# Performance work log

Measured on AMD Instinct MI355X. Metric: run time of the kernel, lower is better.

Reference implementation:

```python
import jax, jax.numpy as jnp
import numpy as np

E, D, H, B = 8, 64, 512, 32768  # n_experts, state_dim, hidden width, batch
IN = D + 3  # x, t, sin(omega*t), cos(omega*t)


def setup_inputs() -> dict:
    key = jax.random.key(0)
    ks = jax.random.split(key, 12)
    s = 0.02
    return {
        "t": jax.random.uniform(ks[0], (1,), dtype=jnp.float32),
        "x": jax.random.normal(ks[1], (B, D), dtype=jnp.float32),
        "expert_weights": jax.random.uniform(ks[2], (B, E), dtype=jnp.float32),
        "omega": jnp.arange(1, E + 1, dtype=jnp.float32),  # omega_i = i+1
        "W1": jax.random.normal(ks[3], (E, H, IN), dtype=jnp.float32) * s,
        "b1": jnp.zeros((E, H), dtype=jnp.float32),
        "W2": jax.random.normal(ks[4], (E, H, H), dtype=jnp.float32) * s,
        "b2": jnp.zeros((E, H), dtype=jnp.float32),
        "W3": jax.random.normal(ks[5], (E, H, H), dtype=jnp.float32) * s,
        "b3": jnp.zeros((E, H), dtype=jnp.float32),
        "W4": jax.random.normal(ks[6], (E, D, H), dtype=jnp.float32) * s,
        "b4": jnp.zeros((E, D), dtype=jnp.float32),
    }


def reference(t, x, expert_weights, omega, W1, b1, W2, b2, W3, b3, W4, b4):
    # Dense path of ExpertODEEnsemble.forward: all experts active.
    nB = x.shape[0]
    tb = jnp.broadcast_to(t, (nB,))                       # (B,)
    wt = omega[:, None] * tb[None, :]                     # (E, B)
    # Per-expert inputs: [x, t, sin(wt), cos(wt)] -> (E, B, D+3)
    xe = jnp.broadcast_to(x[None], (E, nB, D))
    te = jnp.broadcast_to(tb[None, :, None], (E, nB, 1))
    inp = jnp.concatenate([xe, te, jnp.sin(wt)[..., None], jnp.cos(wt)[..., None]], axis=-1)
    h = jnp.tanh(jnp.einsum('ebi,ehi->ebh', inp, W1) + b1[:, None, :])
    h = jnp.tanh(jnp.einsum('ebh,egh->ebg', h, W2) + b2[:, None, :])
    h = jnp.tanh(jnp.einsum('ebh,egh->ebg', h, W3) + b3[:, None, :])
    dyn = jnp.einsum('ebh,edh->ebd', h, W4) + b4[:, None, :]   # (E, B, D)
    # Weighted combine: sum_e w[b,e] * dyn[e,b,:]
    dx_dt = jnp.einsum('be,ebd->bd', expert_weights, dyn)
    return dx_dt
```

## Files before the change

kernel.cpp:

```cpp
#include <hip/hip_runtime.h>
#include <hip/hip_bf16.h>


typedef unsigned short ushort_t;
typedef unsigned int u32;
typedef unsigned long long u64;
typedef __attribute__((ext_vector_type(8))) short short8;
typedef __attribute__((ext_vector_type(4))) float floatx4;
typedef __attribute__((ext_vector_type(16))) float floatx16;
typedef __attribute__((ext_vector_type(4))) int intx4;

#define W1A_OFF 0u
#define W2A_OFF 524288u
#define W3A_OFF 4718592u
#define W4A_OFF 8912896u
#define XB_OFF  9437184u
#define B1E_OFF 13631488u

#define SLOTB 16384
#define SYNC_OFF 147456
#define SMEM_SZ 147552

static __device__ __forceinline__ u32 pk2bf(float a, float b) {
  union { __hip_bfloat162 h; u32 u; } v;
  v.h = __float22bfloat162_rn(make_float2(a, b));
  return v.u;
}

static __device__ __forceinline__ float pade_tanh(float x) {
  float x2 = x * x;
  float num = __builtin_fmaf(x2, __builtin_fmaf(x2, 1.0f, 105.0f), 945.0f);
  float den = __builtin_fmaf(x2, __builtin_fmaf(x2, 15.0f, 420.0f), 945.0f);
  return x * num * __builtin_amdgcn_rcpf(den);
}

static __device__ __forceinline__ floatx16 mfma32(short8 a, short8 b, floatx16 c) {
  return __builtin_amdgcn_mfma_f32_32x32x16_bf16(a, b, c, 0, 0, 0);
}

static __device__ __forceinline__ int slot9(int g, int b) {
  int s = g + b;
  if (s >= 9) s -= 9;
  return s * SLOTB;
}

static __device__ __forceinline__ void waitge(const int* p, int tgt) {
  while (*(volatile const int*)p < tgt) __builtin_amdgcn_s_sleep(1);
  __asm__ __volatile__("" ::: "memory");
}

static __device__ __forceinline__ void waitge4(const int* p, int tgt) {
  for (;;) {
    __asm__ __volatile__("" ::: "memory");
    intx4 v = *(const intx4*)p;
    if (v[0] >= tgt && v[1] >= tgt && v[2] >= tgt && v[3] >= tgt) break;
    __builtin_amdgcn_s_sleep(1);
  }
  __asm__ __volatile__("" ::: "memory");
}

static __device__ __forceinline__ void guard_grp(const int* grp, int w, int base) {
  int tg0 = base + ((0 - w - 1) & 7) + 1;
  int tg1 = base + ((1 - w - 1) & 7) + 1;
  int tg2 = base + ((2 - w - 1) & 7) + 1;
  int tg3 = base + ((3 - w - 1) & 7) + 1;
  int tg4 = base + ((4 - w - 1) & 7) + 1;
  int tg5 = base + ((5 - w - 1) & 7) + 1;
  int tg6 = base + ((6 - w - 1) & 7) + 1;
  int tg7 = base + ((7 - w - 1) & 7) + 1;
  for (;;) {
    __asm__ __volatile__("" ::: "memory");
    intx4 a = *(const intx4*)grp;
    intx4 b = *(const intx4*)(grp + 4);
    if (a[0] >= tg0 && a[1] >= tg1 && a[2] >= tg2 && a[3] >= tg3 &&
        b[0] >= tg4 && b[1] >= tg5 && b[2] >= tg6 && b[3] >= tg7) break;
    __builtin_amdgcn_s_sleep(1);
  }
  __asm__ __volatile__("" ::: "memory");
}

static __device__ __forceinline__ void bump(int* p, int lane) {
  __asm__ __volatile__("s_waitcnt lgkmcnt(0)" ::: "memory");
  if (lane == 0) atomicAdd(p, 1);
}

static __device__ __forceinline__ void bump_sig(int* p, int lane) {
  __builtin_amdgcn_sched_barrier(0);
  if (lane == 0) atomicAdd(p, 1);
}

__global__ __launch_bounds__(256) void prep_kernel(
    const float* __restrict__ t, const float* __restrict__ x,
    const float* __restrict__ omega, const float* __restrict__ W1,
    const float* __restrict__ b1, const float* __restrict__ W2,
    const float* __restrict__ W3, const float* __restrict__ W4,
    char* __restrict__ ws) {
  int i = blockIdx.x * 256 + threadIdx.x;
  if (i < 32768) {
    int e = i >> 12, d = i & 4095;
    int lane = d & 63, q = d >> 6;
    int ol = q & 1, kc = (q >> 1) & 3, w = q >> 3;
    int outr = w * 64 + ol * 32 + (lane & 31);
    int kg = kc * 2 + (lane >> 5);
    const float* s = W1 + (e * 512 + outr) * 67 + kg * 8;
    ((intx4*)(ws + W1A_OFF))[i] = (intx4){
        (int)pk2bf(s[0], s[1]), (int)pk2bf(s[2], s[3]),
        (int)pk2bf(s[4], s[5]), (int)pk2bf(s[6], s[7])};
    return;
  }
  i -= 32768;
  if (i < 262144) {
    int e = i >> 15, d = i & 32767;
    int lane = d & 63, q = d >> 6;
    int ol = q & 1, kc = (q >> 1) & 31, w = q >> 6;
    int outr = w * 64 + ol * 32 + (lane & 31);
    int kg = kc * 2 + (lane >> 5);
    const floatx4* s = (const floatx4*)(W2 + ((e << 9) + outr) * 512 + (kg << 3));
    floatx4 lo = s[0], hi = s[1];
    ((intx4*)(ws + W2A_OFF))[i] = (intx4){
        (int)pk2bf(lo[0], lo[1]), (int)pk2bf(lo[2], lo[3]),
        (int)pk2bf(hi[0], hi[1]), (int)pk2bf(hi[2], hi[3])};
    return;
  }
  i -= 262144;
  if (i < 262144) {
    int e = i >> 15, d = i & 32767;
    int lane = d & 63, q = d >> 6;
    int ol = q & 1, kc = (q >> 1) & 31, w = q >> 6;
    int outr = w * 64 + ol * 32 + (lane & 31);
    int kg = kc * 2 + (lane >> 5);
    const floatx4* s = (const floatx4*)(W3 + ((e << 9) + outr) * 512 + (kg << 3));
    floatx4 lo = s[0], hi = s[1];
    ((intx4*)(ws + W3A_OFF))[i] = (intx4){
        (int)pk2bf(lo[0], lo[1]), (int)pk2bf(lo[2], lo[3]),
        (int)pk2bf(hi[0], hi[1]), (int)pk2bf(hi[2], hi[3])};
    return;
  }
  i -= 262144;
  if (i < 32768) {
    int e = i >> 12, d = i & 4095;
    int lane = d & 63, q = d >> 6;
    int kc = q & 31, o4 = q >> 5;
    int outr = o4 * 32 + (lane & 31);
    int kg = kc * 2 + (lane >> 5);
    const floatx4* s = (const floatx4*)(W4 + ((e << 6) + outr) * 512 + (kg << 3));
    floatx4 lo = s[0], hi = s[1];
    ((intx4*)(ws + W4A_OFF))[i] = (intx4){
        (int)pk2bf(lo[0], lo[1]), (int)pk2bf(lo[2], lo[3]),
        (int)pk2bf(hi[0], hi[1]), (int)pk2bf(hi[2], hi[3])};
    return;
  }
  i -= 32768;
  if (i < 262144) {
    const floatx4* s = (const floatx4*)(x + i * 8);
    floatx4 lo = s[0], hi = s[1];
    ((intx4*)(ws + XB_OFF))[i] = (intx4){
        (int)pk2bf(lo[0], lo[1]), (int)pk2bf(lo[2], lo[3]),
        (int)pk2bf(hi[0], hi[1]), (int)pk2bf(hi[2], hi[3])};
    return;
  }
  i -= 262144;
  if (i < 4096) {
    float tv = t[0];
    int e = i >> 9;
    float om = omega[e];
    ((float*)(ws + B1E_OFF))[i] = b1[i] + tv * W1[i * 67 + 64]
        + sinf(om * tv) * W1[i * 67 + 65] + cosf(om * tv) * W1[i * 67 + 66];
  }
}


static __device__ __forceinline__ void epi_write(
    floatx16 acc[2][4], char* __restrict__ act, int wbyte, int r31, int q1) {
#pragma unroll
  for (int ol = 0; ol < 2; ++ol) {
#pragma unroll
    for (int g = 0; g < 4; ++g) {
      int ko = ol * 4 + g;
      char* base = act + wbyte + (ko >> 1) * 4096
                   + (((ko & 1) * 32 + r31) << 4) + q1 * 8;
#pragma unroll
      for (int nt = 0; nt < 4; ++nt) {
        float v0 = pade_tanh(acc[ol][nt][4 * g + 0]);
        float v1 = pade_tanh(acc[ol][nt][4 * g + 1]);
        float v2 = pade_tanh(acc[ol][nt][4 * g + 2]);
        float v3 = pade_tanh(acc[ol][nt][4 * g + 3]);
        u32 lo = pk2bf(v0, v1), hi = pk2bf(v2, v3);
        *(u64*)(base + nt * 1024) = ((u64)hi << 32) | lo;
      }
    }
  }
}

static __device__ __forceinline__ void mlp_l1(
    char* __restrict__ act, int* pub, int* l4c, int* grp,
    int lane, int w, int q1, int r31,
    const char* __restrict__ Abase, const float* __restrict__ bias,
    const char* __restrict__ xl, int wbyte, int e) {
  const int voff = lane * 16;
  const char* ap = Abase + w * 8192 + voff;

  floatx16 acc[2][4];
#pragma unroll
  for (int ol = 0; ol < 2; ++ol) {
    int fe0 = w * 64 + ol * 32 + 4 * q1;
#pragma unroll
    for (int g = 0; g < 4; ++g) {
      floatx4 bv = *(const floatx4*)(bias + fe0 + 8 * g);
#pragma unroll
      for (int nt = 0; nt < 4; ++nt) {
        acc[ol][nt][4 * g + 0] = bv[0];
        acc[ol][nt][4 * g + 1] = bv[1];
        acc[ol][nt][4 * g + 2] = bv[2];
        acc[ol][nt][4 * g + 3] = bv[3];
      }
    }
  }
  short8 b0 = *(const short8*)(xl);
  short8 b1v = *(const short8*)(xl + 4096);
  short8 b2 = *(const short8*)(xl + 8192);
  short8 b3 = *(const short8*)(xl + 12288);
  short8 a0 = *(const short8*)(ap);
  short8 a1 = *(const short8*)(ap + 1024);

#pragma unroll
  for (int j = 0; j < 4; ++j) {
    int kcn = (j < 3) ? (j + 1) : 3;
    const char* xn = xl + kcn * 32;
    const char* apn = (j < 3) ? (ap + 2048) : ap;
    short8 an0 = *(const short8*)(apn);
    short8 an1 = *(const short8*)(apn + 1024);
    short8 bn0 = *(const short8*)(xn);
    short8 bn1 = *(const short8*)(xn + 4096);
    short8 bn2 = *(const short8*)(xn + 8192);
    short8 bn3 = *(const short8*)(xn + 12288);
    __builtin_amdgcn_s_setprio(1);
    acc[0][0] = mfma32(a0, b0, acc[0][0]);
    acc[0][1] = mfma32(a0, b1v, acc[0][1]);
    acc[0][2] = mfma32(a0, b2, acc[0][2]);
    acc[0][3] = mfma32(a0, b3, acc[0][3]);
    acc[1][0] = mfma32(a1, b0, acc[1][0]);
    acc[1][1] = mfma32(a1, b1v, acc[1][1]);
    acc[1][2] = mfma32(a1, b2, acc[1][2]);
    acc[1][3] = mfma32(a1, b3, acc[1][3]);
    __builtin_amdgcn_s_setprio(0);
    a0 = an0; a1 = an1;
    b0 = bn0; b1v = bn1; b2 = bn2; b3 = bn3;
    ap = apn;
  }
  if (e > 0) {
    if (w < 7) waitge4(l4c + ((w + 1) >> 2) * 4, e);
    else       guard_grp(grp, w, 16 * e - 8);
  }
  epi_write(acc, act, wbyte, r31, q1);
  bump(pub + w, lane);
}

static __device__ __forceinline__ void mlp_mid(
    char* __restrict__ act, int* pub, int* grp, int lane, int w, int q1, int r31,
    const char* __restrict__ Abase, const float* __restrict__ bias,
    int pub_tgt, int rbase9, int wbyte, int gmode, int garg,
    const int* __restrict__ l4p) {
  const int voff = lane * 16;
  const char* spA = Abase + w * 65536 + voff;

  floatx16 acc[2][4];
#pragma unroll
  for (int ol = 0; ol < 2; ++ol) {
    int fe0 = w * 64 + ol * 32 + 4 * q1;
#pragma unroll
    for (int g = 0; g < 4; ++g) {
      floatx4 bv = *(const floatx4*)(bias + fe0 + 8 * g);
#pragma unroll
      for (int nt = 0; nt < 4; ++nt) {
        acc[ol][nt][4 * g + 0] = bv[0];
        acc[ol][nt][4 * g + 1] = bv[1];
        acc[ol][nt][4 * g + 2] = bv[2];
        acc[ol][nt][4 * g + 3] = bv[3];
      }
    }
  }
  const char* gb = act + slot9(w, rbase9) + voff;
  const char* ap = spA + (4 * w) * 2048;
  short8 b0 = *(const short8*)(gb);
  short8 b1v = *(const short8*)(gb + 1024);
  short8 b2 = *(const short8*)(gb + 2048);
  short8 b3 = *(const short8*)(gb + 3072);
  short8 a0 = *(const short8*)(ap);
  short8 a1 = *(const short8*)(ap + 1024);

#pragma unroll 1
  for (int i = 0; i < 8; ++i) {
#pragma unroll
    for (int j = 0; j < 4; ++j) {
      const char* apn;
      const char* gbn = gb;
      const char* bsl;
      if (j < 3) {
        apn = ap + 2048;
        bsl = gb + (j + 1) * 4096;
      } else if (i < 7) {
        int g2 = (w - i - 1) & 7;
        waitge(pub + g2, pub_tgt);
        gbn = act + slot9(g2, rbase9) + voff;
        apn = spA + (4 * g2) * 2048;
        bsl = gbn;
      } else {
        apn = ap; bsl = gb;
      }
      short8 an0 = *(const short8*)(apn);
      short8 an1 = *(const short8*)(apn + 1024);
      short8 bn0 = *(const short8*)(bsl);
      short8 bn1 = *(const short8*)(bsl + 1024);
      short8 bn2 = *(const short8*)(bsl + 2048);
      short8 bn3 = *(const short8*)(bsl + 3072);
      __builtin_amdgcn_s_setprio(1);
      acc[0][0] = mfma32(a0, b0, acc[0][0]);
      acc[0][1] = mfma32(a0, b1v, acc[0][1]);
      acc[0][2] = mfma32(a0, b2, acc[0][2]);
      acc[0][3] = mfma32(a0, b3, acc[0][3]);
      acc[1][0] = mfma32(a1, b0, acc[1][0]);
      acc[1][1] = mfma32(a1, b1v, acc[1][1]);
      acc[1][2] = mfma32(a1, b2, acc[1][2]);
      acc[1][3] = mfma32(a1, b3, acc[1][3]);
      __builtin_amdgcn_s_setprio(0);
      a0 = an0; a1 = an1;
      b0 = bn0; b1v = bn1; b2 = bn2; b3 = bn3;
      ap = apn; gb = gbn;
    }
    bump_sig(grp + w, lane);
  }

  if (gmode == 1)      guard_grp(grp, w, garg);
  else if (gmode == 2) waitge4(l4p, garg);
  epi_write(acc, act, wbyte, r31, q1);
  bump(pub + w, lane);
}

extern "C" __global__ __launch_bounds__(512) void fused_kernel(
    const char* __restrict__ ws, const float* __restrict__ b2,
    const float* __restrict__ b3, const float* __restrict__ b4,
    const float* __restrict__ ew, float* __restrict__ out) {
  extern __shared__ char smem[];
  char* act = smem;
  int* l4c = (int*)(smem + SYNC_OFF);
  int* pub = l4c + 8;
  int* grp = l4c + 16;

  const int t = threadIdx.x, lane = t & 63, w = t >> 6;
  const int q1 = lane >> 5, r31 = lane & 31;
  const int row0 = blockIdx.x << 7;
  const int voff = lane * 16;

  if (t < 24) ((int*)(smem + SYNC_OFF))[t] = 0;
  __syncthreads();

  for (int i = (7 - w) * 7; i > 0; --i) __builtin_amdgcn_s_sleep(1);

  const char* xl = (const char*)ws + XB_OFF + (size_t)row0 * 128
                   + r31 * 128 + q1 * 16;

  const int rt = w & 3, kh = w >> 2;
  const int row_l4 = row0 + rt * 32 + r31;
  floatx16 oacc[2] = {};

  for (int e = 0; e < 8; ++e) {
    int l0 = 3 * e;
    int s1 = (l0 + 1) % 9, s2 = (l0 + 2) % 9, s3 = (l0 + 3) % 9;

    mlp_l1(act, pub, l4c, grp, lane, w, q1, r31,
           (const char*)ws + W1A_OFF + e * 65536,
           (const float*)(ws + B1E_OFF) + e * 512, xl, slot9(w, s1), e);
    mlp_mid(act, pub, grp, lane, w, q1, r31,
            (const char*)ws + W2A_OFF + e * 524288, b2 + e * 512,
            3 * e + 1, s1, slot9(w, s2),
            (w < 7) ? 1 : ((e > 0) ? 2 : 0),
            (w < 7) ? 16 * e : e, l4c);
    mlp_mid(act, pub, grp, lane, w, q1, r31,
            (const char*)ws + W3A_OFF + e * 524288, b3 + e * 512,
            3 * e + 2, s2, slot9(w, s3),
            1, (w < 7) ? 16 * e + 8 : 16 * e, l4c);

    {
      const char* spA4 = (const char*)ws + W4A_OFF + e * 65536 + voff;
      const float sc = ew[row_l4 * 8 + e];
      floatx16 acc4[2] = {};
      int g = 4 * kh + 3;
      waitge(pub + g, 3 * e + 3);
      const char* agb = spA4 + (4 * g) * 1024;
      const char* gb = act + slot9(g, s3) + rt * 1024 + voff;
      short8 a0 = *(const short8*)(agb);
      short8 a1 = *(const short8*)(agb + 32768);
      short8 b = *(const short8*)(gb);
#pragma unroll 1
      for (int gl = 0; gl < 4; ++gl) {
#pragma unroll
        for (int j = 0; j < 4; ++j) {
          const char* agn = agb;
          const char* gbn = gb;
          const char* asl; const char* bsl;
          if (j < 3) {
            asl = agb + (j + 1) * 1024;
            bsl = gb + (j + 1) * 4096;
          } else if (gl < 3) {
            int g2 = g - 1;
            waitge(pub + g2, 3 * e + 3);
            agn = spA4 + (4 * g2) * 1024;
            gbn = act + slot9(g2, s3) + rt * 1024 + voff;
            asl = agn; bsl = gbn;
          } else {
            asl = agb; bsl = gb;
          }
          short8 an0 = *(const short8*)(asl);
          short8 an1 = *(const short8*)(asl + 32768);
          short8 bn = *(const short8*)(bsl);
          __builtin_amdgcn_s_setprio(1);
          acc4[0] = mfma32(a0, b, acc4[0]);
          acc4[1] = mfma32(a1, b, acc4[1]);
          __builtin_amdgcn_s_setprio(0);
          a0 = an0; a1 = an1; b = bn;
          agb = agn; gb = gbn;
        }
        g = g - 1;
      }
      bump_sig(l4c + w, lane);
      if (kh == 0) {
        const float* bp = b4 + e * 64;
#pragma unroll
        for (int ol = 0; ol < 2; ++ol) {
          int fe0 = ol * 32 + 4 * q1;
#pragma unroll
          for (int g2 = 0; g2 < 4; ++g2) {
            floatx4 bv = *(const floatx4*)(bp + fe0 + 8 * g2);
            oacc[ol][4 * g2 + 0] += sc * (acc4[ol][4 * g2 + 0] + bv[0]);
            oacc[ol][4 * g2 + 1] += sc * (acc4[ol][4 * g2 + 1] + bv[1]);
            oacc[ol][4 * g2 + 2] += sc * (acc4[ol][4 * g2 + 2] + bv[2]);
            oacc[ol][4 * g2 + 3] += sc * (acc4[ol][4 * g2 + 3] + bv[3]);
          }
        }
      } else {
#pragma unroll
        for (int ol = 0; ol < 2; ++ol)
#pragma unroll
          for (int i = 0; i < 16; ++i) oacc[ol][i] += sc * acc4[ol][i];
      }
    }
  }

  __syncthreads();
  if (kh == 1) {
#pragma unroll
    for (int ol = 0; ol < 2; ++ol)
#pragma unroll
      for (int g = 0; g < 4; ++g) {
        floatx4 p = {oacc[ol][4 * g + 0], oacc[ol][4 * g + 1],
                     oacc[ol][4 * g + 2], oacc[ol][4 * g + 3]};
        *(floatx4*)(act + rt * 8192 + ol * 4096 + g * 1024 + lane * 16) = p;
      }
  }
  __syncthreads();
  if (kh == 0) {
    float* orow = out + (size_t)row_l4 * 64;
#pragma unroll
    for (int ol = 0; ol < 2; ++ol)
#pragma unroll
      for (int g = 0; g < 4; ++g) {
        floatx4 p = *(const floatx4*)(act + rt * 8192 + ol * 4096 + g * 1024 + lane * 16);
        floatx4 v = {oacc[ol][4 * g + 0] + p[0], oacc[ol][4 * g + 1] + p[1],
                     oacc[ol][4 * g + 2] + p[2], oacc[ol][4 * g + 3] + p[3]};
        *(floatx4*)(orow + ol * 32 + 8 * g + 4 * q1) = v;
      }
  }
}

extern "C" void kernel_launch(void* const* d_in, const int* in_sizes, int n_in,
                              void* d_out, int out_size, void* d_ws, size_t ws_size,
                              hipStream_t stream) {
  const float* t  = (const float*)d_in[0];
  const float* x  = (const float*)d_in[1];
  const float* ew = (const float*)d_in[2];
  const float* om = (const float*)d_in[3];
  const float* W1 = (const float*)d_in[4];
  const float* b1 = (const float*)d_in[5];
  const float* W2 = (const float*)d_in[6];
  const float* b2 = (const float*)d_in[7];
  const float* W3 = (const float*)d_in[8];
  const float* b3 = (const float*)d_in[9];
  const float* W4 = (const float*)d_in[10];
  const float* b4 = (const float*)d_in[11];
  char* ws = (char*)d_ws;
  float* out = (float*)d_out;
  (void)in_sizes; (void)n_in; (void)ws_size; (void)out_size;

  static int smem_set = 0;
  if (!smem_set) {
    hipFuncSetAttribute((const void*)fused_kernel,
                        hipFuncAttributeMaxDynamicSharedMemorySize, SMEM_SZ);
    smem_set = 1;
  }
  prep_kernel<<<3344, 256, 0, stream>>>(t, x, om, W1, b1, W2, W3, W4, ws);
  fused_kernel<<<256, 512, SMEM_SZ, stream>>>(ws, b2, b3, b4, ew, out);
}
```

Measured before the change: 461.3 us.

## Stage x tile into LDS once and shrink activation ring to eight slots

Loads the block's bf16 x tile into LDS once at kernel start with global_load_lds, so layer 1 of every expert reads x from LDS instead of re-reading it from global memory eight times. To free the LDS for this, the activation ring buffer drops from nine slots to eight, using a mask instead of a modulo. The cross-wave guard logic is simplified to match. The smaller ring changes slot reuse distances, which could add stalls or hazards between layers.

```diff
diff --git a/kernel.cpp b/kernel.cpp
--- a/kernel.cpp
+++ b/kernel.cpp
@@ -18,6 +18,7 @@
 #define B1E_OFF 13631488u
 
 #define SLOTB 16384
+#define X_OFF_L 131072
 #define SYNC_OFF 147456
 #define SMEM_SZ 147552
 
@@ -34,14 +35,18 @@
   return x * num * __builtin_amdgcn_rcpf(den);
 }
 
+static __device__ __forceinline__ void ald16(const void* g, void* l) {
+  __builtin_amdgcn_global_load_lds((__attribute__((address_space(1))) void*)g,
+                                   (__attribute__((address_space(3))) void*)l,
+                                   16, 0, 0);
+}
+
 static __device__ __forceinline__ floatx16 mfma32(short8 a, short8 b, floatx16 c) {
   return __builtin_amdgcn_mfma_f32_32x32x16_bf16(a, b, c, 0, 0, 0);
 }
 
-static __device__ __forceinline__ int slot9(int g, int b) {
-  int s = g + b;
-  if (s >= 9) s -= 9;
-  return s * SLOTB;
+static __device__ __forceinline__ int slot8(int g, int b) {
+  return ((g + b) & 7) * SLOTB;
 }
 
 static __device__ __forceinline__ void waitge(const int* p, int tgt) {
@@ -193,10 +198,10 @@
 }
 
 static __device__ __forceinline__ void mlp_l1(
-    char* __restrict__ act, int* pub, int* l4c, int* grp,
-    int lane, int w, int q1, int r31,
+    char* __restrict__ act, const char* __restrict__ xreg,
+    int* pub, int* l4c, int lane, int w, int q1, int r31,
     const char* __restrict__ Abase, const float* __restrict__ bias,
-    const char* __restrict__ xl, int wbyte, int e) {
+    int wbyte, int e) {
   const int voff = lane * 16;
   const char* ap = Abase + w * 8192 + voff;
 
@@ -216,24 +221,25 @@
       }
     }
   }
-  short8 b0 = *(const short8*)(xl);
-  short8 b1v = *(const short8*)(xl + 4096);
-  short8 b2 = *(const short8*)(xl + 8192);
-  short8 b3 = *(const short8*)(xl + 12288);
+  const char* xb0 = xreg + voff;
+  short8 b0 = *(const short8*)(xb0);
+  short8 b1v = *(const short8*)(xb0 + 1024);
+  short8 b2 = *(const short8*)(xb0 + 2048);
+  short8 b3 = *(const short8*)(xb0 + 3072);
   short8 a0 = *(const short8*)(ap);
   short8 a1 = *(const short8*)(ap + 1024);
 
 #pragma unroll
   for (int j = 0; j < 4; ++j) {
-    int kcn = (j < 3) ? (j + 1) : 3;
-    const char* xn = xl + kcn * 32;
+    int jn = (j < 3) ? (j + 1) : 3;
+    const char* xn = xreg + jn * 4096 + voff;
     const char* apn = (j < 3) ? (ap + 2048) : ap;
     short8 an0 = *(const short8*)(apn);
     short8 an1 = *(const short8*)(apn + 1024);
     short8 bn0 = *(const short8*)(xn);
-    short8 bn1 = *(const short8*)(xn + 4096);
-    short8 bn2 = *(const short8*)(xn + 8192);
-    short8 bn3 = *(const short8*)(xn + 12288);
+    short8 bn1 = *(const short8*)(xn + 1024);
+    short8 bn2 = *(const short8*)(xn + 2048);
+    short8 bn3 = *(const short8*)(xn + 3072);
     __builtin_amdgcn_s_setprio(1);
     acc[0][0] = mfma32(a0, b0, acc[0][0]);
     acc[0][1] = mfma32(a0, b1v, acc[0][1]);
@@ -248,10 +254,7 @@
     b0 = bn0; b1v = bn1; b2 = bn2; b3 = bn3;
     ap = apn;
   }
-  if (e > 0) {
-    if (w < 7) waitge4(l4c + ((w + 1) >> 2) * 4, e);
-    else       guard_grp(grp, w, 16 * e - 8);
-  }
+  if (e > 0) waitge4(l4c + ((((w + 1) & 7) >> 2) << 2), e);
   epi_write(acc, act, wbyte, r31, q1);
   bump(pub + w, lane);
 }
@@ -259,8 +262,7 @@
 static __device__ __forceinline__ void mlp_mid(
     char* __restrict__ act, int* pub, int* grp, int lane, int w, int q1, int r31,
     const char* __restrict__ Abase, const float* __restrict__ bias,
-    int pub_tgt, int rbase9, int wbyte, int gmode, int garg,
-    const int* __restrict__ l4p) {
+    int pub_tgt, int rbase, int wbyte, int gbase) {
   const int voff = lane * 16;
   const char* spA = Abase + w * 65536 + voff;
 
@@ -280,7 +282,7 @@
       }
     }
   }
-  const char* gb = act + slot9(w, rbase9) + voff;
+  const char* gb = act + slot8(w, rbase) + voff;
   const char* ap = spA + (4 * w) * 2048;
   short8 b0 = *(const short8*)(gb);
   short8 b1v = *(const short8*)(gb + 1024);
@@ -302,7 +304,7 @@
       } else if (i < 7) {
         int g2 = (w - i - 1) & 7;
         waitge(pub + g2, pub_tgt);
-        gbn = act + slot9(g2, rbase9) + voff;
+        gbn = act + slot8(g2, rbase) + voff;
         apn = spA + (4 * g2) * 2048;
         bsl = gbn;
       } else {
@@ -331,8 +333,7 @@
     bump_sig(grp + w, lane);
   }
 
-  if (gmode == 1)      guard_grp(grp, w, garg);
-  else if (gmode == 2) waitge4(l4p, garg);
+  guard_grp(grp, w, gbase);
   epi_write(acc, act, wbyte, r31, q1);
   bump(pub + w, lane);
 }
@@ -343,6 +344,7 @@
     const float* __restrict__ ew, float* __restrict__ out) {
   extern __shared__ char smem[];
   char* act = smem;
+  char* xreg = smem + X_OFF_L;
   int* l4c = (int*)(smem + SYNC_OFF);
   int* pub = l4c + 8;
   int* grp = l4c + 16;
@@ -353,33 +355,36 @@
   const int voff = lane * 16;
 
   if (t < 24) ((int*)(smem + SYNC_OFF))[t] = 0;
+
+  const ushort_t* xb = (const ushort_t*)(ws + XB_OFF);
+#pragma unroll
+  for (int s = 0; s < 2; ++s) {
+    int u = w + 8 * s, v = u >> 2, nt = u & 3;
+    ald16(xb + (row0 + nt * 32 + r31) * 64 + (2 * v + q1) * 8,
+          xreg + v * 4096 + nt * 1024);
+  }
   __syncthreads();
 
   for (int i = (7 - w) * 7; i > 0; --i) __builtin_amdgcn_s_sleep(1);
-
-  const char* xl = (const char*)ws + XB_OFF + (size_t)row0 * 128
-                   + r31 * 128 + q1 * 16;
 
   const int rt = w & 3, kh = w >> 2;
   const int row_l4 = row0 + rt * 32 + r31;
   floatx16 oacc[2] = {};
 
   for (int e = 0; e < 8; ++e) {
-    int l0 = 3 * e;
-    int s1 = (l0 + 1) % 9, s2 = (l0 + 2) % 9, s3 = (l0 + 3) % 9;
-
-    mlp_l1(act, pub, l4c, grp, lane, w, q1, r31,
+    int b1s = (3 * e + 1) & 7;
+    int b2s = (3 * e + 2) & 7;
+    int b3s = (3 * e + 3) & 7;
+
+    mlp_l1(act, xreg, pub, l4c, lane, w, q1, r31,
            (const char*)ws + W1A_OFF + e * 65536,
-           (const float*)(ws + B1E_OFF) + e * 512, xl, slot9(w, s1), e);
+           (const float*)(ws + B1E_OFF) + e * 512, slot8(w, b1s), e);
     mlp_mid(act, pub, grp, lane, w, q1, r31,
             (const char*)ws + W2A_OFF + e * 524288, b2 + e * 512,
-            3 * e + 1, s1, slot9(w, s2),
-            (w < 7) ? 1 : ((e > 0) ? 2 : 0),
-            (w < 7) ? 16 * e : e, l4c);
+            3 * e + 1, b1s, slot8(w, b2s), 16 * e);
     mlp_mid(act, pub, grp, lane, w, q1, r31,
             (const char*)ws + W3A_OFF + e * 524288, b3 + e * 512,
-            3 * e + 2, s2, slot9(w, s3),
-            1, (w < 7) ? 16 * e + 8 : 16 * e, l4c);
+            3 * e + 2, b2s, slot8(w, b3s), 16 * e + 8);
 
     {
       const char* spA4 = (const char*)ws + W4A_OFF + e * 65536 + voff;
@@ -388,7 +393,7 @@
       int g = 4 * kh + 3;
       waitge(pub + g, 3 * e + 3);
       const char* agb = spA4 + (4 * g) * 1024;
-      const char* gb = act + slot9(g, s3) + rt * 1024 + voff;
+      const char* gb = act + slot8(g, b3s) + rt * 1024 + voff;
       short8 a0 = *(const short8*)(agb);
       short8 a1 = *(const short8*)(agb + 32768);
       short8 b = *(const short8*)(gb);
@@ -406,7 +411,7 @@
             int g2 = g - 1;
             waitge(pub + g2, 3 * e + 3);
             agn = spA4 + (4 * g2) * 1024;
-            gbn = act + slot9(g2, s3) + rt * 1024 + voff;
+            gbn = act + slot8(g2, b3s) + rt * 1024 + voff;
             asl = agn; bsl = gbn;
           } else {
             asl = agb; bsl = gb;
```

New measurement: 427.2 us. 1.08x faster.
